# Performance work log

Measured on AMD Instinct MI355X. Metric: run time of the kernel, lower is better.

Reference implementation:

```python
import jax, jax.numpy as jnp
import numpy as np

PI2 = float(np.pi ** 2)
# freqs3d from __init__: y in arange(-4,4)/8 (len 8, centered), x in arange(5)/8 (rfft half)
_y = np.arange(-4, 4) / 8.0
_x = np.arange(5) / 8.0
_gz, _gy, _gx = np.meshgrid(_y, _y, _x, indexing='ij')
S2 = jnp.asarray(_gx**2 + _gy**2 + _gz**2, dtype=jnp.float32)   # (8,8,5)

def rfft3_center(x):
    x = jnp.fft.ifftshift(x, axes=(-3, -2, -1))
    f = jnp.fft.rfftn(x, axes=(-3, -2, -1))
    return jnp.fft.fftshift(f, axes=(-3, -2))

def irfft3_center(f):
    f = jnp.fft.ifftshift(f, axes=(-3, -2))
    x = jnp.fft.irfftn(f, s=(8, 8, 8), axes=(-3, -2, -1))
    return jnp.fft.fftshift(x, axes=(-3, -2, -1))

def conv3d(x, w, b, stride, pad):
    y = jax.lax.conv_general_dilated(x, w, (stride,) * 3, [(pad, pad)] * 3,
        dimension_numbers=('NCDHW', 'OIDHW', 'NCDHW'))
    return y + b[None, :, None, None, None]

def leaky(x):
    return jnp.where(x >= 0, x, 0.2 * x)

def group_norm(x, G, g, b, eps=1e-5):
    N = x.shape[0]
    xr = x.reshape(N, G, -1)
    m = xr.mean(-1, keepdims=True)
    v = xr.var(-1, keepdims=True)
    xn = ((xr - m) * jax.lax.rsqrt(v + eps)).reshape(x.shape)
    return xn * g[None, :, None, None, None] + b[None, :, None, None, None]

def layer_norm(x, g, b, eps=1e-5):
    m = x.mean(-1, keepdims=True)
    v = x.var(-1, keepdims=True)
    return (x - m) * jax.lax.rsqrt(v + eps) * g + b

def setup_inputs() -> dict:
    key = jax.random.key(0)
    ks = list(jax.random.split(key, 40)); it = iter(ks)
    B = 16
    def nrm(shape, s):
        return jax.random.normal(next(it), shape, jnp.float32) * s
    inp = {}
    inp['img'] = jax.random.uniform(next(it), (B, 64, 64, 64), jnp.float32)
    inp['b_factor'] = jax.random.uniform(next(it), (B * 512,), jnp.float32)
    inp['w0'] = nrm((32, 1, 4, 4, 4), 0.1);    inp['b0c'] = jnp.zeros((32,))
    inp['g1'] = jnp.ones((32,));               inp['be1'] = jnp.zeros((32,))
    inp['w1'] = nrm((64, 32, 4, 4, 4), 0.05);  inp['b1c'] = jnp.zeros((64,))
    inp['g2'] = jnp.ones((64,));               inp['be2'] = jnp.zeros((64,))
    inp['w2'] = nrm((128, 64, 4, 4, 4), 0.04); inp['b2c'] = jnp.zeros((128,))
    inp['g3'] = jnp.ones((128,));              inp['be3'] = jnp.zeros((128,))
    inp['wu'] = nrm((256, 128, 1, 1, 1), 0.08); inp['bu'] = jnp.zeros((256,))
    inp['pos_emb'] = nrm((512, 256), 1.0)
    inp['lndg'] = jnp.ones((256,)); inp['lndb'] = jnp.zeros((256,))
    inp['lnpg'] = jnp.ones((256,)); inp['lnpb'] = jnp.zeros((256,))
    L = 8
    inp['Wq'] = nrm((L, 256, 256), 0.02); inp['bq'] = jnp.zeros((L, 256))
    inp['Wk'] = nrm((L, 256, 256), 0.02); inp['bk'] = jnp.zeros((L, 256))
    inp['Wv'] = nrm((L, 256, 256), 0.02); inp['bv'] = jnp.zeros((L, 256))
    inp['Wo'] = nrm((L, 256, 256), 0.02); inp['bo'] = jnp.zeros((L, 256))
    inp['l1g'] = jnp.ones((L, 256)); inp['l1b'] = jnp.zeros((L, 256))
    inp['l2g'] = jnp.ones((L, 256)); inp['l2b'] = jnp.zeros((L, 256))
    inp['W1'] = nrm((L, 256, 1024), 0.02); inp['bf1'] = jnp.zeros((L, 1024))
    inp['W2'] = nrm((L, 1024, 256), 0.02); inp['bf2'] = jnp.zeros((L, 256))
    return inp

def reference(img, b_factor, w0, b0c, g1, be1, w1, b1c, g2, be2, w2, b2c, g3, be3,
              wu, bu, pos_emb, lndg, lndb, lnpg, lnpb,
              Wq, bq, Wk, bk, Wv, bv, Wo, bo, l1g, l1b, l2g, l2b, W1, bf1, W2, bf2):
    B = img.shape[0]
    # unfold (B,64,64,64) into B*512 subvolumes of 8^3 (all patches active for this input)
    p = img.reshape(B, 8, 8, 8, 8, 8, 8).transpose(0, 1, 3, 5, 2, 4, 6)
    p = p.reshape(B * 512, 1, 8, 8, 8)
    # FFT-domain b-factor blurring (bfactor_blurring)
    f = rfft3_center(p)
    f = f * jnp.exp(-S2 * (4.0 * b_factor)[:, None, None, None, None] * PI2)
    p = irfft3_center(f)
    # conv encoder: 8^3 -> 4^3 -> 2^3 -> 1^3
    d = group_norm(leaky(conv3d(p, w0, b0c, 2, 1)), 4, g1, be1)
    d = group_norm(leaky(conv3d(d, w1, b1c, 2, 1)), 2, g2, be2)
    d = group_norm(leaky(conv3d(d, w2, b2c, 2, 1)), 1, g3, be3)
    u = conv3d(d, wu, bu, 1, 0).reshape(B, 512, 256)
    x = layer_norm(u, lndg, lndb) + layer_norm(pos_emb, lnpg, lnpb)[None]
    H, hd = 8, 32
    scale = 1.0 / float(np.sqrt(hd))
    for i in range(8):
        h = layer_norm(x, l1g[i], l1b[i])
        q = (h @ Wq[i] + bq[i]).reshape(B, 512, H, hd)
        k = (h @ Wk[i] + bk[i]).reshape(B, 512, H, hd)
        v = (h @ Wv[i] + bv[i]).reshape(B, 512, H, hd)
        a = jax.nn.softmax(jnp.einsum('bqhd,bkhd->bhqk', q, k) * scale, axis=-1)
        o = jnp.einsum('bhqk,bkhd->bqhd', a, v).reshape(B, 512, 256)
        x = x + (o @ Wo[i] + bo[i])
        h = layer_norm(x, l2g[i], l2b[i])
        x = x + (jax.nn.gelu(h @ W1[i] + bf1[i]) @ W2[i] + bf2[i])
    return x
```

## Files before the change

kernel.cpp:

```cpp
#include <hip/hip_runtime.h>
#include <hip/hip_bf16.h>

#define PI2F 9.869604401089358f

typedef __attribute__((ext_vector_type(8))) short bf16x8;
typedef __attribute__((ext_vector_type(4))) float f32x4;

#define GLOAD16(g, l) __builtin_amdgcn_global_load_lds( \
    (const __attribute__((address_space(1))) void*)(g), \
    (__attribute__((address_space(3))) void*)(l), 16, 0, 0)

__device__ inline unsigned short f2b(float v) {
    union { float f; unsigned u; } x; x.f = v;
    unsigned r = x.u + 0x7fffu + ((x.u >> 16) & 1u);
    return (unsigned short)(r >> 16);
}

__device__ inline float gelu_tanh(float v) {
    float u = 0.7978845608028654f * (v + 0.044715f * v * v * v);
    float th = 1.f - 2.f / (1.f + __expf(2.f * u));
    return 0.5f * v * (1.f + th);
}

__global__ __launch_bounds__(256) void k_blur_conv0(
    const float* __restrict__ img, const float* __restrict__ bfac,
    const float* __restrict__ w0, const float* __restrict__ b0c,
    const float* __restrict__ g1, const float* __restrict__ be1,
    unsigned short* __restrict__ d0)
{
    __shared__ float pa[512], pb[512], hsm[8];
    __shared__ unsigned short pbb[512];
    __shared__ unsigned short w0b[32][72];
    __shared__ float d0s[64 * 33];
    __shared__ float2 gstat[4];
    const int t = threadIdx.x, blk = blockIdx.x;
    const int b = blk >> 9, rem = blk & 511;
    const int zh = rem >> 6, yh = (rem >> 3) & 7, xh = rem & 7;

    #pragma unroll
    for (int i = 0; i < 2; i++) {
        int v = t + 256 * i;
        int z = v >> 6, y = (v >> 3) & 7, x = v & 7;
        pa[v] = img[(((size_t)(b * 8 + zh) * 8 + z) * 64 + yh * 8 + y) * 64 + xh * 8 + x];
    }
    #pragma unroll
    for (int i = 0; i < 8; i++) {
        int idx = i * 256 + t;
        w0b[idx >> 6][idx & 63] = f2b(w0[idx]);
    }
    if (t < 8) {
        float bf = bfac[blk];
        float c = bf * PI2F * (1.0f / 16.0f);
        float gk1 = __expf(-c), gk2 = __expf(-4.f * c), gk3 = __expf(-9.f * c), gk4 = __expf(-16.f * c);
        float d = (float)t;
        float h = 1.f + 2.f * (gk1 * cosf(0.7853981633974483f * d)
                             + gk2 * cosf(1.5707963267948966f * d)
                             + gk3 * cosf(2.356194490192345f * d))
                      + gk4 * cosf(3.141592653589793f * d);
        hsm[t] = 0.125f * h;
    }
    __syncthreads();
    #pragma unroll
    for (int i = 0; i < 2; i++) {
        int v = t + 256 * i; int x = v & 7; int base = v & ~7;
        float s = 0.f;
        #pragma unroll
        for (int m = 0; m < 8; m++) s += hsm[(x - m) & 7] * pa[base + m];
        pb[v] = s;
    }
    __syncthreads();
    #pragma unroll
    for (int i = 0; i < 2; i++) {
        int v = t + 256 * i; int y = (v >> 3) & 7; int base = (v & ~63) | (v & 7);
        float s = 0.f;
        #pragma unroll
        for (int m = 0; m < 8; m++) s += hsm[(y - m) & 7] * pb[base + m * 8];
        pa[v] = s;
    }
    __syncthreads();
    #pragma unroll
    for (int i = 0; i < 2; i++) {
        int v = t + 256 * i; int z = v >> 6; int base = v & 63;
        float s = 0.f;
        #pragma unroll
        for (int m = 0; m < 8; m++) s += hsm[(z - m) & 7] * pa[base + m * 64];
        pb[v] = s;
        pbb[v] = f2b(s);
    }
    __syncthreads();
    const int wid = t >> 6, lane = t & 63;
    const int lr = lane & 15, lk8 = (lane >> 4) * 8;
    {
        const int vox = wid * 16 + lr;
        const int szb = 2 * (vox >> 4) - 1, syb = 2 * ((vox >> 2) & 3) - 1, sxb = 2 * (vox & 3) - 1;
        f32x4 acc0 = {}, acc1 = {};
        #pragma unroll
        for (int ks = 0; ks < 2; ks++) {
            bf16x8 a;
            #pragma unroll
            for (int j = 0; j < 8; j++) {
                int tap = ks * 32 + lk8 + j;
                int sz = szb + (tap >> 4), sy = syb + ((tap >> 2) & 3), sx = sxb + (tap & 3);
                bool ok = (unsigned)sz < 8u && (unsigned)sy < 8u && (unsigned)sx < 8u;
                a[j] = ok ? (short)pbb[sz * 64 + sy * 8 + sx] : (short)0;
            }
            bf16x8 b0 = *(const bf16x8*)&w0b[lr][ks * 32 + lk8];
            bf16x8 b1 = *(const bf16x8*)&w0b[16 + lr][ks * 32 + lk8];
            acc0 = __builtin_amdgcn_mfma_f32_16x16x32_bf16(a, b0, acc0, 0, 0, 0);
            acc1 = __builtin_amdgcn_mfma_f32_16x16x32_bf16(a, b1, acc1, 0, 0, 0);
        }
        const float bA = b0c[lr], bB = b0c[16 + lr];
        #pragma unroll
        for (int r = 0; r < 4; r++) {
            int crow = wid * 16 + (lane >> 4) * 4 + r;
            float v0 = acc0[r] + bA; v0 = v0 >= 0.f ? v0 : 0.2f * v0;
            float v1 = acc1[r] + bB; v1 = v1 >= 0.f ? v1 : 0.2f * v1;
            d0s[crow * 33 + lr] = v0;
            d0s[crow * 33 + 16 + lr] = v1;
        }
    }
    __syncthreads();
    {
        int g = wid;
        float s = 0.f, sq = 0.f;
        #pragma unroll
        for (int cc = 0; cc < 8; cc++) { float v = d0s[lane * 33 + g * 8 + cc]; s += v; sq += v * v; }
        #pragma unroll
        for (int m = 1; m < 64; m <<= 1) { s += __shfl_xor(s, m, 64); sq += __shfl_xor(sq, m, 64); }
        if (lane == 0) {
            float mean = s * (1.f / 512.f);
            float var = sq * (1.f / 512.f) - mean * mean;
            gstat[g] = make_float2(mean, rsqrtf(var + 1e-5f));
        }
    }
    __syncthreads();
    size_t obase = (size_t)blk * 2048;
    #pragma unroll
    for (int i = 0; i < 8; i++) {
        int oi = t + 256 * i;
        int c = oi >> 6, vox = oi & 63;
        float2 st = gstat[oi >> 9];
        d0[obase + oi] = f2b((d0s[vox * 33 + c] - st.x) * st.y * g1[c] + be1[c]);
    }
}

__global__ __launch_bounds__(256) void k_prep_all(
    const float* __restrict__ w1, const float* __restrict__ w2, const float* __restrict__ wu,
    const float* __restrict__ b1c,
    const float* __restrict__ Wq, const float* __restrict__ Wk, const float* __restrict__ Wv,
    const float* __restrict__ bq, const float* __restrict__ bk, const float* __restrict__ bv,
    const float* __restrict__ Wo, const float* __restrict__ W1, const float* __restrict__ W2,
    unsigned short* __restrict__ w1T, unsigned short* __restrict__ w2T,
    unsigned short* __restrict__ wuT, float* __restrict__ b1x,
    unsigned short* __restrict__ WqkvT, float* __restrict__ bqkv,
    unsigned short* __restrict__ WoT, unsigned short* __restrict__ W1T, unsigned short* __restrict__ W2T)
{
    const int blk = blockIdx.x, t = threadIdx.x;
    if (blk < 4096) {
        int idx = blk * 256 + t;
        int n = idx >> 11, k = idx & 2047;
        int oc = n >> 3, vox = n & 7;
        int oz = vox >> 2, oy = (vox >> 1) & 1, ox = vox & 1;
        int ci = k >> 6, sp = k & 63;
        int sz = sp >> 4, sy = (sp >> 2) & 3, sx = sp & 3;
        int kz = sz + 1 - 2 * oz, ky = sy + 1 - 2 * oy, kx = sx + 1 - 2 * ox;
        float v = 0.f;
        if ((unsigned)kz < 4u && (unsigned)ky < 4u && (unsigned)kx < 4u)
            v = w1[(size_t)oc * 2048 + ci * 64 + kz * 16 + ky * 4 + kx];
        w1T[idx] = f2b(v);
    } else if (blk < 4352) {
        int idx = (blk - 4096) * 256 + t;
        int n = idx >> 9, k = idx & 511;
        int ci = k >> 3, v = k & 7;
        int z = v >> 2, y = (v >> 1) & 1, x = v & 1;
        w2T[idx] = f2b(w2[(size_t)n * 4096 + ci * 64 + (z + 1) * 16 + (y + 1) * 4 + (x + 1)]);
    } else if (blk < 4480) {
        int idx = (blk - 4352) * 256 + t;
        wuT[idx] = f2b(wu[idx]);
    } else if (blk < 4482) {
        int idx = (blk - 4480) * 256 + t;
        b1x[idx] = b1c[idx >> 3];
    } else if (blk < 10626) {
        int task = blk - 4482;
        int l = task / 768, n = task % 768;
        int sel = n >> 8, col = n & 255;
        const float* W = sel == 0 ? Wq : sel == 1 ? Wk : Wv;
        const float* bb = sel == 0 ? bq : sel == 1 ? bk : bv;
        WqkvT[((size_t)l * 768 + n) * 256 + t] = f2b(W[(size_t)l * 65536 + (size_t)t * 256 + col]);
        if (t == 0) bqkv[l * 768 + n] = bb[l * 256 + col];
    } else if (blk < 12674) {
        int gid = (blk - 10626) * 256 + t;
        int l = gid >> 16, w = gid & 65535;
        int n = w >> 8, k = w & 255;
        WoT[gid] = f2b(Wo[(size_t)l * 65536 + (size_t)k * 256 + n]);
    } else if (blk < 20866) {
        int gid = (blk - 12674) * 256 + t;
        int l = gid >> 18, w = gid & 262143;
        int n = w >> 8, k = w & 255;
        W1T[gid] = f2b(W1[(size_t)l * 262144 + (size_t)k * 1024 + n]);
    } else {
        int gid = (blk - 20866) * 256 + t;
        int l = gid >> 18, w = gid & 262143;
        int n = w >> 10, k = w & 1023;
        W2T[gid] = f2b(W2[(size_t)l * 262144 + (size_t)k * 256 + n]);
    }
}

template<int BM>
__global__ __launch_bounds__(256) void k_gemm_bf16(
    const unsigned short* __restrict__ A, const unsigned short* __restrict__ WT,
    const float* __restrict__ bias, const float* __restrict__ res,
    void* __restrict__ Cout, int NXB, int N, int K, int act, int obf)
{
    constexpr int MREP = BM / 32;
    __shared__ unsigned short Ash[BM][64];
    __shared__ unsigned short Bsh[64][64];
    const int t = threadIdx.x;
    const int lb = blockIdx.x;
    const int xcd = lb & 7, j = lb >> 3;
    const int gy = xcd * 8 + j / NXB, gx = j % NXB;
    const int c0 = gx * 64;
    const int r0 = gy * BM;
    const int wid = t >> 6, lane = t & 63;
    const int wr = wid >> 1, wc = wid & 1;
    const int lrow = lane & 15, lk = (lane >> 4) * 8;
    const int xsw = (lrow & 7) << 3;
    const int srcsw = ((lane & 7) ^ (lane >> 3)) << 3;
    f32x4 acc[MREP][2] = {};
    for (int k0 = 0; k0 < K; k0 += 64) {
        __syncthreads();
        {
            const unsigned short* ga = A + (size_t)(r0 + wid * (BM / 4) + (lane >> 3)) * K + k0 + srcsw;
            unsigned short* la = &Ash[wid * (BM / 4)][0];
            #pragma unroll
            for (int i = 0; i < BM / 32; i++)
                GLOAD16(ga + (size_t)(i * 8) * K, la + i * 8 * 64);
        }
        {
            const unsigned short* gb = WT + (size_t)(c0 + wid * 16 + (lane >> 3)) * K + k0 + srcsw;
            unsigned short* lbp = &Bsh[wid * 16][0];
            #pragma unroll
            for (int i = 0; i < 2; i++)
                GLOAD16(gb + (size_t)(i * 8) * K, lbp + i * 8 * 64);
        }
        __syncthreads();
        #pragma unroll
        for (int ks = 0; ks < 2; ks++) {
            bf16x8 b0 = *(const bf16x8*)&Bsh[wc * 32 + lrow][(ks * 32 + lk) ^ xsw];
            bf16x8 b1 = *(const bf16x8*)&Bsh[wc * 32 + 16 + lrow][(ks * 32 + lk) ^ xsw];
            #pragma unroll
            for (int m = 0; m < MREP; m++) {
                bf16x8 a = *(const bf16x8*)&Ash[wr * (BM / 2) + m * 16 + lrow][(ks * 32 + lk) ^ xsw];
                acc[m][0] = __builtin_amdgcn_mfma_f32_16x16x32_bf16(a, b0, acc[m][0], 0, 0, 0);
                acc[m][1] = __builtin_amdgcn_mfma_f32_16x16x32_bf16(a, b1, acc[m][1], 0, 0, 0);
            }
        }
    }
    const int rbase = r0 + wr * (BM / 2) + (lane >> 4) * 4;
    #pragma unroll
    for (int n = 0; n < 2; n++) {
        const int col = c0 + wc * 32 + n * 16 + lrow;
        const float bv = bias[col];
        #pragma unroll
        for (int m = 0; m < MREP; m++) {
            #pragma unroll
            for (int r = 0; r < 4; r++) {
                float v = acc[m][n][r] + bv;
                if (act == 1) v = gelu_tanh(v);
                else if (act == 2) v = v >= 0.f ? v : 0.2f * v;
                size_t off = (size_t)(rbase + m * 16 + r) * N + col;
                if (res) v += res[off];
                if (obf) ((unsigned short*)Cout)[off] = f2b(v);
                else ((float*)Cout)[off] = v;
            }
        }
    }
}

__global__ __launch_bounds__(512) void k_gemm_gn(
    const unsigned short* __restrict__ A, const unsigned short* __restrict__ WT,
    const float* __restrict__ bias, const float* __restrict__ g3, const float* __restrict__ be3,
    unsigned short* __restrict__ out)
{
    __shared__ __align__(16) char smem[23040];
    unsigned short (*Ash)[72] = (unsigned short(*)[72])smem;
    unsigned short (*Bsh)[72] = (unsigned short(*)[72])(smem + 4608);
    float (*vals)[136] = (float(*)[136])smem;
    const int t = threadIdx.x;
    const int r0 = blockIdx.x * 32;
    const int wid = t >> 6, lane = t & 63;
    const int mrow = wid >> 2, colq = wid & 3;
    const int lr = lane & 15, lk8 = (lane >> 4) * 8;
    f32x4 acc[2] = {};
    for (int k0 = 0; k0 < 512; k0 += 64) {
        __syncthreads();
        if (t < 256) {
            int f = t * 8;
            int r = f >> 6, kk = f & 63;
            *(bf16x8*)&Ash[r][kk] = *(const bf16x8*)(A + (size_t)(r0 + r) * 512 + k0 + kk);
        }
        #pragma unroll
        for (int i = 0; i < 2; i++) {
            int f = (i * 512 + t) * 8;
            int r = f >> 6, kk = f & 63;
            *(bf16x8*)&Bsh[r][kk] = *(const bf16x8*)(WT + (size_t)r * 512 + k0 + kk);
        }
        __syncthreads();
        #pragma unroll
        for (int ks = 0; ks < 2; ks++) {
            bf16x8 a = *(const bf16x8*)&Ash[mrow * 16 + lr][ks * 32 + lk8];
            #pragma unroll
            for (int nf = 0; nf < 2; nf++) {
                bf16x8 bb = *(const bf16x8*)&Bsh[colq * 32 + nf * 16 + lr][ks * 32 + lk8];
                acc[nf] = __builtin_amdgcn_mfma_f32_16x16x32_bf16(a, bb, acc[nf], 0, 0, 0);
            }
        }
    }
    __syncthreads();
    #pragma unroll
    for (int nf = 0; nf < 2; nf++) {
        int col = colq * 32 + nf * 16 + lr;
        float bv = bias[col];
        #pragma unroll
        for (int r = 0; r < 4; r++) {
            int row = mrow * 16 + (lane >> 4) * 4 + r;
            float v = acc[nf][r] + bv;
            vals[row][col] = v >= 0.f ? v : 0.2f * v;
        }
    }
    __syncthreads();
    const int row = t >> 4, cc0 = (t & 15) * 8;
    float s = 0.f, sq = 0.f;
    #pragma unroll
    for (int j = 0; j < 8; j++) {
        float v = vals[row][cc0 + j];
        s += v; sq += v * v;
    }
    s += __shfl_xor(s, 1); sq += __shfl_xor(sq, 1);
    s += __shfl_xor(s, 2); sq += __shfl_xor(sq, 2);
    s += __shfl_xor(s, 4); sq += __shfl_xor(sq, 4);
    s += __shfl_xor(s, 8); sq += __shfl_xor(sq, 8);
    float mean = s * (1.f / 128.f);
    float rs = rsqrtf(sq * (1.f / 128.f) - mean * mean + 1e-5f);
    ushort4 o[2];
    #pragma unroll
    for (int h = 0; h < 2; h++) {
        #pragma unroll
        for (int j = 0; j < 4; j++) {
            int col = cc0 + h * 4 + j;
            float v = (vals[row][col] - mean) * rs * g3[col] + be3[col];
            ((unsigned short*)&o[h])[j] = f2b(v);
        }
    }
    *(ushort4*)(out + (size_t)(r0 + row) * 128 + cc0) = o[0];
    *(ushort4*)(out + (size_t)(r0 + row) * 128 + cc0 + 4) = o[1];
}

__global__ __launch_bounds__(512) void k_gemm_ln(
    const unsigned short* __restrict__ A, const unsigned short* __restrict__ WT,
    const float* __restrict__ bias, const float* __restrict__ res,
    const float* __restrict__ lng, const float* __restrict__ lnb,
    float* __restrict__ xnew, unsigned short* __restrict__ h, int K)
{
    __shared__ __align__(16) char smem[36864];
    unsigned short (*Ash)[64] = (unsigned short(*)[64])smem;
    unsigned short (*Bsh)[64] = (unsigned short(*)[64])(smem + 4096);
    float (*vals)[264] = (float(*)[264])smem;
    const int t = threadIdx.x;
    const int r0 = blockIdx.x * 32;
    const int wid = t >> 6, lane = t & 63;
    const int lrow = lane & 15, lk8 = (lane >> 4) * 8;
    const int xsw = (lrow & 7) << 3;
    const int srcsw = ((lane & 7) ^ (lane >> 3)) << 3;
    f32x4 acc[2][2] = {};
    for (int k0 = 0; k0 < K; k0 += 64) {
        __syncthreads();
        if (wid < 4) {
            GLOAD16(A + (size_t)(r0 + wid * 8 + (lane >> 3)) * K + k0 + srcsw, &Ash[wid * 8][0]);
        }
        {
            const unsigned short* gb = WT + (size_t)(wid * 32 + (lane >> 3)) * K + k0 + srcsw;
            unsigned short* lbp = &Bsh[wid * 32][0];
            #pragma unroll
            for (int i = 0; i < 4; i++)
                GLOAD16(gb + (size_t)(i * 8) * K, lbp + i * 8 * 64);
        }
        __syncthreads();
        #pragma unroll
        for (int ks = 0; ks < 2; ks++) {
            bf16x8 a0 = *(const bf16x8*)&Ash[lrow][(ks * 32 + lk8) ^ xsw];
            bf16x8 a1 = *(const bf16x8*)&Ash[16 + lrow][(ks * 32 + lk8) ^ xsw];
            #pragma unroll
            for (int nf = 0; nf < 2; nf++) {
                bf16x8 bfr = *(const bf16x8*)&Bsh[wid * 32 + nf * 16 + lrow][(ks * 32 + lk8) ^ xsw];
                acc[0][nf] = __builtin_amdgcn_mfma_f32_16x16x32_bf16(a0, bfr, acc[0][nf], 0, 0, 0);
                acc[1][nf] = __builtin_amdgcn_mfma_f32_16x16x32_bf16(a1, bfr, acc[1][nf], 0, 0, 0);
            }
        }
    }
    __syncthreads();
    #pragma unroll
    for (int m = 0; m < 2; m++)
        #pragma unroll
        for (int nf = 0; nf < 2; nf++) {
            int col = wid * 32 + nf * 16 + lrow;
            float bv = bias[col];
            #pragma unroll
            for (int r = 0; r < 4; r++) {
                int row = m * 16 + (lane >> 4) * 4 + r;
                vals[row][col] = acc[m][nf][r] + bv + res[(size_t)(r0 + row) * 256 + col];
            }
        }
    __syncthreads();
    const int row = t >> 4, c4 = (t & 15) * 4;
    float s = 0.f, sq = 0.f;
    #pragma unroll
    for (int j = 0; j < 4; j++) {
        float4 v4 = *(const float4*)&vals[row][c4 + j * 64];
        s += v4.x + v4.y + v4.z + v4.w;
        sq += v4.x * v4.x + v4.y * v4.y + v4.z * v4.z + v4.w * v4.w;
    }
    s += __shfl_xor(s, 1); sq += __shfl_xor(sq, 1);
    s += __shfl_xor(s, 2); sq += __shfl_xor(sq, 2);
    s += __shfl_xor(s, 4); sq += __shfl_xor(sq, 4);
    s += __shfl_xor(s, 8); sq += __shfl_xor(sq, 8);
    float mean = s * (1.f / 256.f);
    float rs = rsqrtf(sq * (1.f / 256.f) - mean * mean + 1e-5f);
    const size_t gbase = (size_t)(r0 + row) * 256;
    #pragma unroll
    for (int j = 0; j < 4; j++) {
        int col = c4 + j * 64;
        float4 v4 = *(const float4*)&vals[row][col];
        *(float4*)(xnew + gbase + col) = v4;
        if (lng) {
            float4 g4 = *(const float4*)(lng + col);
            float4 b4 = *(const float4*)(lnb + col);
            ushort4 o;
            o.x = f2b((v4.x - mean) * rs * g4.x + b4.x);
            o.y = f2b((v4.y - mean) * rs * g4.y + b4.y);
            o.z = f2b((v4.z - mean) * rs * g4.z + b4.z);
            o.w = f2b((v4.w - mean) * rs * g4.w + b4.w);
            *(ushort4*)(h + gbase + col) = o;
        }
    }
}

__global__ __launch_bounds__(256) void k_gn2(
    const float* __restrict__ din, const float* __restrict__ g2, const float* __restrict__ be2,
    unsigned short* __restrict__ dout)
{
    const int t = threadIdx.x;
    const int w = t >> 6, lane = t & 63;
    const int p = blockIdx.x * 2 + (w >> 1), g = w & 1;
    float4 v = ((const float4*)(din + (size_t)p * 512 + g * 256))[lane];
    float s = v.x + v.y + v.z + v.w;
    float sq = v.x * v.x + v.y * v.y + v.z * v.z + v.w * v.w;
    #pragma unroll
    for (int m = 1; m < 64; m <<= 1) { s += __shfl_xor(s, m, 64); sq += __shfl_xor(sq, m, 64); }
    float mean = s * (1.f / 256.f);
    float rs = rsqrtf(sq * (1.f / 256.f) - mean * mean + 1e-5f);
    int oc = g * 32 + (lane >> 1);
    float gg = g2[oc], bb = be2[oc];
    ushort4 o;
    o.x = f2b((v.x - mean) * rs * gg + bb);
    o.y = f2b((v.y - mean) * rs * gg + bb);
    o.z = f2b((v.z - mean) * rs * gg + bb);
    o.w = f2b((v.w - mean) * rs * gg + bb);
    ((ushort4*)(dout + (size_t)p * 512 + g * 256))[lane] = o;
}

__global__ __launch_bounds__(256) void k_lnpos(
    const float* __restrict__ u, const float* __restrict__ pos,
    const float* __restrict__ lndg, const float* __restrict__ lndb,
    const float* __restrict__ lnpg, const float* __restrict__ lnpb,
    const float* __restrict__ l1g0, const float* __restrict__ l1b0,
    float* __restrict__ xb, unsigned short* __restrict__ hb)
{
    const int t = threadIdx.x;
    const int row = blockIdx.x * 4 + (t >> 6);
    const int lane = t & 63;
    float4 v = ((const float4*)(u + (size_t)row * 256))[lane];
    float4 w = ((const float4*)(pos + (size_t)(row & 511) * 256))[lane];
    float s = v.x + v.y + v.z + v.w;
    float sq = v.x * v.x + v.y * v.y + v.z * v.z + v.w * v.w;
    float sp = w.x + w.y + w.z + w.w;
    float qp = w.x * w.x + w.y * w.y + w.z * w.z + w.w * w.w;
    #pragma unroll
    for (int m = 1; m < 64; m <<= 1) {
        s += __shfl_xor(s, m, 64); sq += __shfl_xor(sq, m, 64);
        sp += __shfl_xor(sp, m, 64); qp += __shfl_xor(qp, m, 64);
    }
    float mu = s * (1.f / 256.f), ru = rsqrtf(sq * (1.f / 256.f) - mu * mu + 1e-5f);
    float mp = sp * (1.f / 256.f), rp = rsqrtf(qp * (1.f / 256.f) - mp * mp + 1e-5f);
    float4 ga = ((const float4*)lndg)[lane], ba = ((const float4*)lndb)[lane];
    float4 gp = ((const float4*)lnpg)[lane], bp = ((const float4*)lnpb)[lane];
    float4 o;
    o.x = (v.x - mu) * ru * ga.x + ba.x + (w.x - mp) * rp * gp.x + bp.x;
    o.y = (v.y - mu) * ru * ga.y + ba.y + (w.y - mp) * rp * gp.y + bp.y;
    o.z = (v.z - mu) * ru * ga.z + ba.z + (w.z - mp) * rp * gp.z + bp.z;
    o.w = (v.w - mu) * ru * ga.w + ba.w + (w.w - mp) * rp * gp.w + bp.w;
    ((float4*)(xb + (size_t)row * 256))[lane] = o;
    float s2 = o.x + o.y + o.z + o.w;
    float q2 = o.x * o.x + o.y * o.y + o.z * o.z + o.w * o.w;
    #pragma unroll
    for (int m = 1; m < 64; m <<= 1) { s2 += __shfl_xor(s2, m, 64); q2 += __shfl_xor(q2, m, 64); }
    float mu2 = s2 * (1.f / 256.f), r2 = rsqrtf(q2 * (1.f / 256.f) - mu2 * mu2 + 1e-5f);
    float4 g4 = ((const float4*)l1g0)[lane], b4 = ((const float4*)l1b0)[lane];
    ushort4 ho;
    ho.x = f2b((o.x - mu2) * r2 * g4.x + b4.x);
    ho.y = f2b((o.y - mu2) * r2 * g4.y + b4.y);
    ho.z = f2b((o.z - mu2) * r2 * g4.z + b4.z);
    ho.w = f2b((o.w - mu2) * r2 * g4.w + b4.w);
    ((ushort4*)(hb + (size_t)row * 256))[lane] = ho;
}

__global__ __launch_bounds__(256) void k_attn3(
    const unsigned short* __restrict__ qkv, unsigned short* __restrict__ og)
{
    __shared__ unsigned short Ks[64][36];
    __shared__ unsigned short Vt[32][72];
    __shared__ unsigned short Pt[4][16][72];
    const int t = threadIdx.x;
    const int bid = blockIdx.x;
    const int b = bid >> 6, hh = (bid >> 3) & 7, qt = bid & 7;
    const int wid = t >> 6, lane = t & 63;
    const int lr = lane & 15, lk8 = (lane >> 4) * 8;
    const int qrow = b * 512 + qt * 64 + wid * 16 + lr;
    const bf16x8 qf = *(const bf16x8*)(qkv + (size_t)qrow * 768 + hh * 32 + lk8);
    f32x4 O0 = {}, O1 = {};
    float mreg[4] = { -1e30f, -1e30f, -1e30f, -1e30f };
    float lreg[4] = {};
    const float scale = 0.17677669529663687f;
    for (int kv0 = 0; kv0 < 512; kv0 += 64) {
        __syncthreads();
        {
            int kvr = t >> 2, dd = (t & 3) * 8;
            size_t base = (size_t)(b * 512 + kv0 + kvr) * 768 + hh * 32;
            *(bf16x8*)&Ks[kvr][dd] = *(const bf16x8*)(qkv + base + 256 + dd);
            bf16x8 v8 = *(const bf16x8*)(qkv + base + 512 + dd);
            #pragma unroll
            for (int j = 0; j < 8; j++) Vt[dd + j][kvr] = (unsigned short)v8[j];
        }
        __syncthreads();
        f32x4 st[4];
        #pragma unroll
        for (int tt = 0; tt < 4; tt++) {
            bf16x8 kf = *(const bf16x8*)&Ks[tt * 16 + lr][lk8];
            st[tt] = __builtin_amdgcn_mfma_f32_16x16x32_bf16(qf, kf, (f32x4){}, 0, 0, 0);
        }
        float mnew[4], csc[4], psum[4];
        #pragma unroll
        for (int r = 0; r < 4; r++) {
            st[0][r] *= scale; st[1][r] *= scale; st[2][r] *= scale; st[3][r] *= scale;
            float mx = fmaxf(fmaxf(st[0][r], st[1][r]), fmaxf(st[2][r], st[3][r]));
            mx = fmaxf(mx, __shfl_xor(mx, 1));
            mx = fmaxf(mx, __shfl_xor(mx, 2));
            mx = fmaxf(mx, __shfl_xor(mx, 4));
            mx = fmaxf(mx, __shfl_xor(mx, 8));
            mnew[r] = fmaxf(mreg[r], mx);
            csc[r] = __expf(mreg[r] - mnew[r]);
            mreg[r] = mnew[r];
            psum[r] = 0.f;
        }
        #pragma unroll
        for (int tt = 0; tt < 4; tt++)
            #pragma unroll
            for (int r = 0; r < 4; r++) {
                float p = __expf(st[tt][r] - mnew[r]);
                st[tt][r] = p;
                psum[r] += p;
            }
        #pragma unroll
        for (int r = 0; r < 4; r++) {
            psum[r] += __shfl_xor(psum[r], 1);
            psum[r] += __shfl_xor(psum[r], 2);
            psum[r] += __shfl_xor(psum[r], 4);
            psum[r] += __shfl_xor(psum[r], 8);
            lreg[r] = lreg[r] * csc[r] + psum[r];
            O0[r] *= csc[r]; O1[r] *= csc[r];
        }
        #pragma unroll
        for (int tt = 0; tt < 4; tt++)
            #pragma unroll
            for (int r = 0; r < 4; r++)
                Pt[wid][(lane >> 4) * 4 + r][tt * 16 + lr] = f2b(st[tt][r]);
        #pragma unroll
        for (int half = 0; half < 2; half++) {
            bf16x8 pa  = *(const bf16x8*)&Pt[wid][lr][half * 32 + lk8];
            bf16x8 vlo = *(const bf16x8*)&Vt[lr][half * 32 + lk8];
            bf16x8 vhi = *(const bf16x8*)&Vt[16 + lr][half * 32 + lk8];
            O0 = __builtin_amdgcn_mfma_f32_16x16x32_bf16(pa, vlo, O0, 0, 0, 0);
            O1 = __builtin_amdgcn_mfma_f32_16x16x32_bf16(pa, vhi, O1, 0, 0, 0);
        }
    }
    #pragma unroll
    for (int r = 0; r < 4; r++) {
        float inv = 1.f / lreg[r];
        size_t orow = (size_t)(b * 512 + qt * 64 + wid * 16 + (lane >> 4) * 4 + r) * 256 + hh * 32;
        og[orow + lr] = f2b(O0[r] * inv);
        og[orow + 16 + lr] = f2b(O1[r] * inv);
    }
}

extern "C" void kernel_launch(void* const* d_in, const int* in_sizes, int n_in,
                              void* d_out, int out_size, void* d_ws, size_t ws_size,
                              hipStream_t stream)
{
    const float* img  = (const float*)d_in[0];
    const float* bfac = (const float*)d_in[1];
    const float* w0  = (const float*)d_in[2];  const float* b0c = (const float*)d_in[3];
    const float* g1  = (const float*)d_in[4];  const float* be1 = (const float*)d_in[5];
    const float* w1  = (const float*)d_in[6];  const float* b1c = (const float*)d_in[7];
    const float* g2  = (const float*)d_in[8];  const float* be2 = (const float*)d_in[9];
    const float* w2  = (const float*)d_in[10]; const float* b2c = (const float*)d_in[11];
    const float* g3  = (const float*)d_in[12]; const float* be3 = (const float*)d_in[13];
    const float* wu  = (const float*)d_in[14]; const float* bu  = (const float*)d_in[15];
    const float* pos = (const float*)d_in[16];
    const float* lndg = (const float*)d_in[17]; const float* lndb = (const float*)d_in[18];
    const float* lnpg = (const float*)d_in[19]; const float* lnpb = (const float*)d_in[20];
    const float* Wq = (const float*)d_in[21]; const float* bq = (const float*)d_in[22];
    const float* Wk = (const float*)d_in[23]; const float* bk = (const float*)d_in[24];
    const float* Wv = (const float*)d_in[25]; const float* bv = (const float*)d_in[26];
    const float* Wo = (const float*)d_in[27]; const float* bo = (const float*)d_in[28];
    const float* l1g = (const float*)d_in[29]; const float* l1b = (const float*)d_in[30];
    const float* l2g = (const float*)d_in[31]; const float* l2b = (const float*)d_in[32];
    const float* W1 = (const float*)d_in[33]; const float* bf1 = (const float*)d_in[34];
    const float* W2 = (const float*)d_in[35]; const float* bf2 = (const float*)d_in[36];

    float* ws = (float*)d_ws;
    unsigned short* d0b   = (unsigned short*)(ws);
    float*          d1raw = ws + 8388608;
    unsigned short* d1b   = (unsigned short*)(ws + 12582912);
    float*          xb    = ws + 14680064;
    unsigned short* w1T   = (unsigned short*)(ws + 16777216);
    unsigned short* w2T   = (unsigned short*)(ws + 17301504);
    unsigned short* wuTb  = (unsigned short*)(ws + 17334272);
    unsigned short* WqkvT = (unsigned short*)(ws + 17350656);
    unsigned short* WoT   = (unsigned short*)(ws + 18137088);
    unsigned short* W1T   = (unsigned short*)(ws + 18399232);
    unsigned short* W2T   = (unsigned short*)(ws + 19447808);
    float*          b1x   = ws + 20496384;
    float*          bqkv  = ws + 20496896;
    unsigned short* d2b   = (unsigned short*)(ws + 1048576);
    float*          ub    = ws + 1572864;
    unsigned short* hb    = (unsigned short*)(ws);
    unsigned short* qkvb  = (unsigned short*)(ws + 1048576);
    unsigned short* obb   = (unsigned short*)(ws + 4194304);
    unsigned short* m1b   = (unsigned short*)(ws + 5242880);
    float* xout = (float*)d_out;

    k_prep_all<<<29058, 256, 0, stream>>>(w1, w2, wu, b1c, Wq, Wk, Wv, bq, bk, bv, Wo, W1, W2,
                                          w1T, w2T, wuTb, b1x, WqkvT, bqkv, WoT, W1T, W2T);

    k_blur_conv0<<<8192, 256, 0, stream>>>(img, bfac, w0, b0c, g1, be1, d0b);
    k_gemm_bf16<128><<<8 * 64, 256, 0, stream>>>(d0b, w1T, b1x, nullptr, d1raw, 8, 512, 2048, 2, 0);
    k_gn2<<<4096, 256, 0, stream>>>(d1raw, g2, be2, d1b);
    k_gemm_gn<<<256, 512, 0, stream>>>(d1b, w2T, b2c, g3, be3, d2b);
    k_gemm_bf16<128><<<4 * 64, 256, 0, stream>>>(d2b, wuTb, bu, nullptr, ub, 4, 256, 128, 0, 0);
    k_lnpos<<<2048, 256, 0, stream>>>(ub, pos, lndg, lndb, lnpg, lnpb, l1g, l1b, xb, hb);

    for (int i = 0; i < 8; i++) {
        k_gemm_bf16<128><<<12 * 64, 256, 0, stream>>>(hb, WqkvT + (size_t)i * 196608, bqkv + i * 768, nullptr, qkvb, 12, 768, 256, 0, 1);
        k_attn3<<<1024, 256, 0, stream>>>(qkvb, obb);
        k_gemm_ln<<<256, 512, 0, stream>>>(obb, WoT + (size_t)i * 65536, bo + i * 256, xb,
                                           l2g + i * 256, l2b + i * 256, xb, hb, 256);
        k_gemm_bf16<128><<<16 * 64, 256, 0, stream>>>(hb, W1T + (size_t)i * 262144, bf1 + i * 1024, nullptr, m1b, 16, 1024, 256, 1, 1);
        if (i < 7) {
            k_gemm_ln<<<256, 512, 0, stream>>>(m1b, W2T + (size_t)i * 262144, bf2 + i * 256, xb,
                                               l1g + (i + 1) * 256, l1b + (i + 1) * 256, xb, hb, 1024);
        } else {
            k_gemm_ln<<<256, 512, 0, stream>>>(m1b, W2T + (size_t)i * 262144, bf2 + i * 256, xb,
                                               nullptr, nullptr, xout, nullptr, 1024);
        }
    }
}
```

Before: 827.3 us.

## Fuse FFN up-projection, GELU, down-projection and LayerNorm into one kernel

Replaces the separate W1 GEMM (with GELU) and the W2 GEMM+residual+LayerNorm kernels with a single kernel. Each block keeps a 32-row tile and holds the 1024-wide GELU intermediate in shared memory, so the m1 activation buffer never goes to global memory and one launch per layer is removed. In exchange, the kernel uses about 80KB of LDS per block, runs only 256 blocks, and reads both weight matrices straight from global memory without LDS staging, which may limit occupancy and MFMA throughput.

New measurement: 830.5 us. Within noise of the previous version (+0.4%).

```diff
diff --git a/kernel.cpp b/kernel.cpp
--- a/kernel.cpp
+++ b/kernel.cpp
@@ -445,6 +445,116 @@
     }
 }
 
+__global__ __launch_bounds__(512) void k_ffn(
+    const unsigned short* __restrict__ A, const unsigned short* __restrict__ W1T,
+    const float* __restrict__ bf1, const unsigned short* __restrict__ W2T,
+    const float* __restrict__ bf2, const float* __restrict__ res,
+    const float* __restrict__ lng, const float* __restrict__ lnb,
+    float* __restrict__ xnew, unsigned short* __restrict__ h)
+{
+    __shared__ __align__(16) char smem[16384 + 66048];
+    unsigned short* Asm = (unsigned short*)smem;
+    unsigned short* Gsm = (unsigned short*)(smem + 16384);
+    float (*vals)[264] = (float(*)[264])(smem + 16384);
+    const int t = threadIdx.x;
+    const int r0 = blockIdx.x * 32;
+    const int wid = t >> 6, lane = t & 63;
+    const int lrow = lane & 15, lk8 = (lane >> 4) * 8;
+    #pragma unroll
+    for (int i = 0; i < 2; i++) {
+        int fb = wid * 1024 + i * 512;
+        int row = (fb >> 8) + (lane >> 5);
+        int colb = (lane & 31) * 8;
+        int gcol = colb ^ ((row & 7) << 3);
+        GLOAD16(A + (size_t)(r0 + row) * 256 + gcol, Asm + fb);
+    }
+    __syncthreads();
+    {
+        f32x4 acc[2][8] = {};
+        for (int k0 = 0; k0 < 256; k0 += 32) {
+            const int r1 = lrow, r2 = lrow + 16;
+            bf16x8 a0 = *(const bf16x8*)&Asm[r1 * 256 + ((k0 + lk8) ^ ((r1 & 7) << 3))];
+            bf16x8 a1 = *(const bf16x8*)&Asm[r2 * 256 + ((k0 + lk8) ^ ((r2 & 7) << 3))];
+            #pragma unroll
+            for (int nf = 0; nf < 8; nf++) {
+                bf16x8 b = *(const bf16x8*)(W1T + (size_t)(wid * 128 + nf * 16 + lrow) * 256 + k0 + lk8);
+                acc[0][nf] = __builtin_amdgcn_mfma_f32_16x16x32_bf16(a0, b, acc[0][nf], 0, 0, 0);
+                acc[1][nf] = __builtin_amdgcn_mfma_f32_16x16x32_bf16(a1, b, acc[1][nf], 0, 0, 0);
+            }
+        }
+        #pragma unroll
+        for (int nf = 0; nf < 8; nf++) {
+            int col = wid * 128 + nf * 16 + lrow;
+            float bv = bf1[col];
+            #pragma unroll
+            for (int m = 0; m < 2; m++)
+                #pragma unroll
+                for (int r = 0; r < 4; r++) {
+                    int row = m * 16 + (lane >> 4) * 4 + r;
+                    Gsm[row * 1032 + (col ^ ((row & 7) << 3))] = f2b(gelu_tanh(acc[m][nf][r] + bv));
+                }
+        }
+    }
+    __syncthreads();
+    f32x4 acc2[2][2] = {};
+    for (int k0 = 0; k0 < 1024; k0 += 32) {
+        const int r1 = lrow, r2 = lrow + 16;
+        bf16x8 a0 = *(const bf16x8*)&Gsm[r1 * 1032 + ((k0 + lk8) ^ ((r1 & 7) << 3))];
+        bf16x8 a1 = *(const bf16x8*)&Gsm[r2 * 1032 + ((k0 + lk8) ^ ((r2 & 7) << 3))];
+        #pragma unroll
+        for (int nf = 0; nf < 2; nf++) {
+            bf16x8 b = *(const bf16x8*)(W2T + (size_t)(wid * 32 + nf * 16 + lrow) * 1024 + k0 + lk8);
+            acc2[0][nf] = __builtin_amdgcn_mfma_f32_16x16x32_bf16(a0, b, acc2[0][nf], 0, 0, 0);
+            acc2[1][nf] = __builtin_amdgcn_mfma_f32_16x16x32_bf16(a1, b, acc2[1][nf], 0, 0, 0);
+        }
+    }
+    __syncthreads();
+    #pragma unroll
+    for (int m = 0; m < 2; m++)
+        #pragma unroll
+        for (int nf = 0; nf < 2; nf++) {
+            int col = wid * 32 + nf * 16 + lrow;
+            float bv = bf2[col];
+            #pragma unroll
+            for (int r = 0; r < 4; r++) {
+                int row = m * 16 + (lane >> 4) * 4 + r;
+                vals[row][col] = acc2[m][nf][r] + bv + res[(size_t)(r0 + row) * 256 + col];
+            }
+        }
+    __syncthreads();
+    const int row = t >> 4, c4 = (t & 15) * 4;
+    float s = 0.f, sq = 0.f;
+    #pragma unroll
+    for (int j = 0; j < 4; j++) {
+        float4 v4 = *(const float4*)&vals[row][c4 + j * 64];
+        s += v4.x + v4.y + v4.z + v4.w;
+        sq += v4.x * v4.x + v4.y * v4.y + v4.z * v4.z + v4.w * v4.w;
+    }
+    s += __shfl_xor(s, 1); sq += __shfl_xor(sq, 1);
+    s += __shfl_xor(s, 2); sq += __shfl_xor(sq, 2);
+    s += __shfl_xor(s, 4); sq += __shfl_xor(sq, 4);
+    s += __shfl_xor(s, 8); sq += __shfl_xor(sq, 8);
+    float mean = s * (1.f / 256.f);
+    float rs = rsqrtf(sq * (1.f / 256.f) - mean * mean + 1e-5f);
+    const size_t gbase = (size_t)(r0 + row) * 256;
+    #pragma unroll
+    for (int j = 0; j < 4; j++) {
+        int col = c4 + j * 64;
+        float4 v4 = *(const float4*)&vals[row][col];
+        *(float4*)(xnew + gbase + col) = v4;
+        if (lng) {
+            float4 g4 = *(const float4*)(lng + col);
+            float4 b4 = *(const float4*)(lnb + col);
+            ushort4 o;
+            o.x = f2b((v4.x - mean) * rs * g4.x + b4.x);
+            o.y = f2b((v4.y - mean) * rs * g4.y + b4.y);
+            o.z = f2b((v4.z - mean) * rs * g4.z + b4.z);
+            o.w = f2b((v4.w - mean) * rs * g4.w + b4.w);
+            *(ushort4*)(h + gbase + col) = o;
+        }
+    }
+}
+
 __global__ __launch_bounds__(256) void k_gn2(
     const float* __restrict__ din, const float* __restrict__ g2, const float* __restrict__ be2,
     unsigned short* __restrict__ dout)
@@ -646,7 +756,6 @@
     unsigned short* hb    = (unsigned short*)(ws);
     unsigned short* qkvb  = (unsigned short*)(ws + 1048576);
     unsigned short* obb   = (unsigned short*)(ws + 4194304);
-    unsigned short* m1b   = (unsigned short*)(ws + 5242880);
     float* xout = (float*)d_out;
 
     k_prep_all<<<29058, 256, 0, stream>>>(w1, w2, wu, b1c, Wq, Wk, Wv, bq, bk, bv, Wo, W1, W2,
@@ -664,13 +773,14 @@
         k_attn3<<<1024, 256, 0, stream>>>(qkvb, obb);
         k_gemm_ln<<<256, 512, 0, stream>>>(obb, WoT + (size_t)i * 65536, bo + i * 256, xb,
                                            l2g + i * 256, l2b + i * 256, xb, hb, 256);
-        k_gemm_bf16<128><<<16 * 64, 256, 0, stream>>>(hb, W1T + (size_t)i * 262144, bf1 + i * 1024, nullptr, m1b, 16, 1024, 256, 1, 1);
         if (i < 7) {
-            k_gemm_ln<<<256, 512, 0, stream>>>(m1b, W2T + (size_t)i * 262144, bf2 + i * 256, xb,
-                                               l1g + (i + 1) * 256, l1b + (i + 1) * 256, xb, hb, 1024);
+            k_ffn<<<256, 512, 0, stream>>>(hb, W1T + (size_t)i * 262144, bf1 + i * 1024,
+                                           W2T + (size_t)i * 262144, bf2 + i * 256, xb,
+                                           l1g + (i + 1) * 256, l1b + (i + 1) * 256, xb, hb);
         } else {
-            k_gemm_ln<<<256, 512, 0, stream>>>(m1b, W2T + (size_t)i * 262144, bf2 + i * 256, xb,
-                                               nullptr, nullptr, xout, nullptr, 1024);
-        }
-    }
-}
+            k_ffn<<<256, 512, 0, stream>>>(hb, W1T + (size_t)i * 262144, bf1 + i * 1024,
+                                           W2T + (size_t)i * 262144, bf2 + i * 256, xb,
+                                           nullptr, nullptr, xout, nullptr);
+        }
+    }
+}
```

## Double-buffer LDS tiles in bf16 GEMM and GEMM+LayerNorm kernels

Applied to the files above, without the earlier changes.

Both MFMA GEMM kernels now keep two LDS buffers. Each iteration issues the asynchronous global-to-LDS load for the next K tile before computing on the current one. This aims to hide global load latency behind MFMA work and cuts the barriers per K step from two to one. The cost is double the shared memory, which in the fused GEMM+LayerNorm kernel grows to 72KB and may reduce how many blocks fit on a CU.

After: 801.6 us. 3.1% less time.

```diff
diff --git a/kernel.cpp b/kernel.cpp
--- a/kernel.cpp
+++ b/kernel.cpp
@@ -213,8 +213,8 @@
     void* __restrict__ Cout, int NXB, int N, int K, int act, int obf)
 {
     constexpr int MREP = BM / 32;
-    __shared__ unsigned short Ash[BM][64];
-    __shared__ unsigned short Bsh[64][64];
+    __shared__ unsigned short Ash[2][BM][64];
+    __shared__ unsigned short Bsh[2][64][64];
     const int t = threadIdx.x;
     const int lb = blockIdx.x;
     const int xcd = lb & 7, j = lb >> 3;
@@ -226,35 +226,39 @@
     const int lrow = lane & 15, lk = (lane >> 4) * 8;
     const int xsw = (lrow & 7) << 3;
     const int srcsw = ((lane & 7) ^ (lane >> 3)) << 3;
+
+    auto stage = [&](int k0, int bsel) {
+        const unsigned short* ga = A + (size_t)(r0 + wid * (BM / 4) + (lane >> 3)) * K + k0 + srcsw;
+        unsigned short* la = &Ash[bsel][wid * (BM / 4)][0];
+        #pragma unroll
+        for (int i = 0; i < BM / 32; i++)
+            GLOAD16(ga + (size_t)(i * 8) * K, la + i * 8 * 64);
+        const unsigned short* gb = WT + (size_t)(c0 + wid * 16 + (lane >> 3)) * K + k0 + srcsw;
+        unsigned short* lbp = &Bsh[bsel][wid * 16][0];
+        #pragma unroll
+        for (int i = 0; i < 2; i++)
+            GLOAD16(gb + (size_t)(i * 8) * K, lbp + i * 8 * 64);
+    };
+
     f32x4 acc[MREP][2] = {};
+    stage(0, 0);
+    __syncthreads();
+    int cur = 0;
     for (int k0 = 0; k0 < K; k0 += 64) {
-        __syncthreads();
-        {
-            const unsigned short* ga = A + (size_t)(r0 + wid * (BM / 4) + (lane >> 3)) * K + k0 + srcsw;
-            unsigned short* la = &Ash[wid * (BM / 4)][0];
-            #pragma unroll
-            for (int i = 0; i < BM / 32; i++)
-                GLOAD16(ga + (size_t)(i * 8) * K, la + i * 8 * 64);
-        }
-        {
-            const unsigned short* gb = WT + (size_t)(c0 + wid * 16 + (lane >> 3)) * K + k0 + srcsw;
-            unsigned short* lbp = &Bsh[wid * 16][0];
-            #pragma unroll
-            for (int i = 0; i < 2; i++)
-                GLOAD16(gb + (size_t)(i * 8) * K, lbp + i * 8 * 64);
-        }
-        __syncthreads();
+        if (k0 + 64 < K) stage(k0 + 64, cur ^ 1);
         #pragma unroll
         for (int ks = 0; ks < 2; ks++) {
-            bf16x8 b0 = *(const bf16x8*)&Bsh[wc * 32 + lrow][(ks * 32 + lk) ^ xsw];
-            bf16x8 b1 = *(const bf16x8*)&Bsh[wc * 32 + 16 + lrow][(ks * 32 + lk) ^ xsw];
+            bf16x8 b0 = *(const bf16x8*)&Bsh[cur][wc * 32 + lrow][(ks * 32 + lk) ^ xsw];
+            bf16x8 b1 = *(const bf16x8*)&Bsh[cur][wc * 32 + 16 + lrow][(ks * 32 + lk) ^ xsw];
             #pragma unroll
             for (int m = 0; m < MREP; m++) {
-                bf16x8 a = *(const bf16x8*)&Ash[wr * (BM / 2) + m * 16 + lrow][(ks * 32 + lk) ^ xsw];
+                bf16x8 a = *(const bf16x8*)&Ash[cur][wr * (BM / 2) + m * 16 + lrow][(ks * 32 + lk) ^ xsw];
                 acc[m][0] = __builtin_amdgcn_mfma_f32_16x16x32_bf16(a, b0, acc[m][0], 0, 0, 0);
                 acc[m][1] = __builtin_amdgcn_mfma_f32_16x16x32_bf16(a, b1, acc[m][1], 0, 0, 0);
             }
         }
+        __syncthreads();
+        cur ^= 1;
     }
     const int rbase = r0 + wr * (BM / 2) + (lane >> 4) * 4;
     #pragma unroll
@@ -362,9 +366,7 @@
     const float* __restrict__ lng, const float* __restrict__ lnb,
     float* __restrict__ xnew, unsigned short* __restrict__ h, int K)
 {
-    __shared__ __align__(16) char smem[36864];
-    unsigned short (*Ash)[64] = (unsigned short(*)[64])smem;
-    unsigned short (*Bsh)[64] = (unsigned short(*)[64])(smem + 4096);
+    __shared__ __align__(16) char smem[73728];
     float (*vals)[264] = (float(*)[264])smem;
     const int t = threadIdx.x;
     const int r0 = blockIdx.x * 32;
@@ -372,20 +374,27 @@
     const int lrow = lane & 15, lk8 = (lane >> 4) * 8;
     const int xsw = (lrow & 7) << 3;
     const int srcsw = ((lane & 7) ^ (lane >> 3)) << 3;
+
+    auto stage = [&](int k0, int bsel) {
+        unsigned short (*Ash)[64] = (unsigned short(*)[64])(smem + bsel * 4096);
+        unsigned short (*Bsh)[64] = (unsigned short(*)[64])(smem + 8192 + bsel * 32768);
+        if (wid < 4)
+            GLOAD16(A + (size_t)(r0 + wid * 8 + (lane >> 3)) * K + k0 + srcsw, &Ash[wid * 8][0]);
+        const unsigned short* gb = WT + (size_t)(wid * 32 + (lane >> 3)) * K + k0 + srcsw;
+        unsigned short* lbp = &Bsh[wid * 32][0];
+        #pragma unroll
+        for (int i = 0; i < 4; i++)
+            GLOAD16(gb + (size_t)(i * 8) * K, lbp + i * 8 * 64);
+    };
+
     f32x4 acc[2][2] = {};
+    stage(0, 0);
+    __syncthreads();
+    int cur = 0;
     for (int k0 = 0; k0 < K; k0 += 64) {
-        __syncthreads();
-        if (wid < 4) {
-            GLOAD16(A + (size_t)(r0 + wid * 8 + (lane >> 3)) * K + k0 + srcsw, &Ash[wid * 8][0]);
-        }
-        {
-            const unsigned short* gb = WT + (size_t)(wid * 32 + (lane >> 3)) * K + k0 + srcsw;
-            unsigned short* lbp = &Bsh[wid * 32][0];
-            #pragma unroll
-            for (int i = 0; i < 4; i++)
-                GLOAD16(gb + (size_t)(i * 8) * K, lbp + i * 8 * 64);
-        }
-        __syncthreads();
+        if (k0 + 64 < K) stage(k0 + 64, cur ^ 1);
+        unsigned short (*Ash)[64] = (unsigned short(*)[64])(smem + cur * 4096);
+        unsigned short (*Bsh)[64] = (unsigned short(*)[64])(smem + 8192 + cur * 32768);
         #pragma unroll
         for (int ks = 0; ks < 2; ks++) {
             bf16x8 a0 = *(const bf16x8*)&Ash[lrow][(ks * 32 + lk8) ^ xsw];
@@ -397,8 +406,9 @@
                 acc[1][nf] = __builtin_amdgcn_mfma_f32_16x16x32_bf16(a1, bfr, acc[1][nf], 0, 0, 0);
             }
         }
-    }
-    __syncthreads();
+        __syncthreads();
+        cur ^= 1;
+    }
     #pragma unroll
     for (int m = 0; m < 2; m++)
         #pragma unroll
```
